# Optimization experiments

Hardware: AMD Instinct MI355X
Metric: run time of the kernel (lower is better)

Reference implementation:

```python
import jax, jax.numpy as jnp
import numpy as np

B, S, D, H = 2, 2048, 1024, 16
RANK = int(D * 0.2)  # 204, per decom(): rank = int(min(a,b)*ratio_LR)
HEAD = D // H


def setup_inputs() -> dict:
    key = jax.random.key(0)
    ks = jax.random.split(key, 16)
    s_in = 1.0 / np.sqrt(D)
    s_r = 1.0 / np.sqrt(RANK)
    inp = {
        'q': jax.random.normal(ks[0], (B, S, D), jnp.float32),
        'k': jax.random.normal(ks[1], (B, S, D), jnp.float32),
        'v': jax.random.normal(ks[2], (B, S, D), jnp.float32),
    }
    names = ['q', 'k', 'v', 'o']
    for i, n in enumerate(names):
        inp[f'V{n}'] = jax.random.uniform(ks[3 + 3 * i], (RANK, D), jnp.float32, -s_in, s_in)
        inp[f'U{n}'] = jax.random.uniform(ks[4 + 3 * i], (D, RANK), jnp.float32, -s_r, s_r)
        inp[f'b{n}'] = jax.random.uniform(ks[5 + 3 * i], (D,), jnp.float32, -s_r, s_r)
    return inp


def _factorized(x, Vw, Uw, b):
    # x @ V^T @ U^T + b  (low-rank linear: Linear(D->rank, no bias) then Linear(rank->D, bias))
    return jnp.einsum('bsr,dr->bsd', jnp.einsum('bsd,rd->bsr', x, Vw), Uw) + b


def _split_heads(x):
    # [B,S,D] -> [B,H,S,HEAD]
    return x.reshape(B, S, H, HEAD).transpose(0, 2, 1, 3)


def reference(q, k, v, Vq, Uq, bq, Vk, Uk, bk, Vv, Uv, bv, Vo, Uo, bo):
    qh = _split_heads(_factorized(q, Vq, Uq, bq))
    kh = _split_heads(_factorized(k, Vk, Uk, bk))
    vh = _split_heads(_factorized(v, Vv, Uv, bv))
    temperature = jnp.asarray(HEAD, jnp.float32) ** 0.5
    scores = jnp.einsum('bhqd,bhkd->bhqk', qh, kh) / temperature
    causal = jnp.tril(jnp.ones((S, S), bool))  # recreated each call in original
    scores = jnp.where(causal, scores, -jnp.inf)
    attn = jax.nn.softmax(scores, axis=-1)  # [B,H,S,S]
    out = jnp.einsum('bhqk,bhkd->bhqd', attn, vh)
    out = out.transpose(0, 2, 1, 3).reshape(B, S, D)
    out = _factorized(out, Vo, Uo, bo)
    # original returns attn flattened over batch*heads
    return out, attn.reshape(B * H, S, S)
```

## Files before the change

kernel.cpp:

```cpp
#include <hip/hip_runtime.h>
#include <stdint.h>

#define BB   2
#define SS   2048
#define DD   1024
#define NH   16
#define RK   204
#define RKP  256
#define HDIM 64
#define BH   (BB*NH)

typedef __attribute__((ext_vector_type(8))) short short8;
typedef __attribute__((ext_vector_type(4))) float f32x4;
typedef unsigned short u16;
typedef unsigned int   u32;

#define NEGBIG (-1e30f)

static __device__ __forceinline__ u16 f2bf(float f) {
    union { float f; u32 u; } v; v.f = f;
    u32 u = v.u;
    return (u16)((u + 0x7fffu + ((u >> 16) & 1u)) >> 16);
}
static __device__ __forceinline__ u32 pack2(float lo, float hi) {
    return (u32)f2bf(lo) | ((u32)f2bf(hi) << 16);
}

__global__ void cvt_bf16_k(const float* __restrict__ in, u16* __restrict__ out, int n4) {
    int i = blockIdx.x * blockDim.x + threadIdx.x;
    if (i < n4) {
        float4 f = ((const float4*)in)[i];
        u32 lo = pack2(f.x, f.y), hi = pack2(f.z, f.w);
        ((uint2*)out)[i] = make_uint2(lo, hi);
    }
}

__global__ void cvt_pad_u_k(const float* __restrict__ in, u16* __restrict__ out) {
    int i = blockIdx.x * blockDim.x + threadIdx.x;
    if (i >= DD * RKP) return;
    int row = i >> 8, col = i & (RKP - 1);
    out[i] = (col < RK) ? f2bf(in[row * RK + col]) : (u16)0;
}

template<int A_F32, int OUT_F32, int HAS_BIAS, int OUT_VT>
__global__ __launch_bounds__(256)
void gemm_nt_k(const void* __restrict__ Ap, int lda,
               const u16* __restrict__ Bp, int ldb, int nrowsB,
               const float* __restrict__ bias,
               void* __restrict__ Cp, int ldc, int K)
{
    __shared__ __align__(16) u16 As[64*72];
    __shared__ __align__(16) u16 Bs[64*72];
    const int row0 = blockIdx.x * 64;
    const int col0 = blockIdx.y * 64;
    const int t = threadIdx.x;
    const int w = t >> 6, lane = t & 63, quad = lane >> 4, l16 = lane & 15;
    const int r = t >> 2, seg = t & 3;

    f32x4 acc0 = 0.f, acc1 = 0.f, acc2 = 0.f, acc3 = 0.f;

    for (int k0 = 0; k0 < K; k0 += 64) {
        __syncthreads();
        if (A_F32) {
            const float* ga = (const float*)Ap + (size_t)(row0 + r) * lda + k0 + seg*16;
            float4 f0 = ((const float4*)ga)[0];
            float4 f1 = ((const float4*)ga)[1];
            float4 f2 = ((const float4*)ga)[2];
            float4 f3 = ((const float4*)ga)[3];
            uint4 s0 = { pack2(f0.x,f0.y), pack2(f0.z,f0.w), pack2(f1.x,f1.y), pack2(f1.z,f1.w) };
            uint4 s1 = { pack2(f2.x,f2.y), pack2(f2.z,f2.w), pack2(f3.x,f3.y), pack2(f3.z,f3.w) };
            *(uint4*)(As + r*72 + seg*16)     = s0;
            *(uint4*)(As + r*72 + seg*16 + 8) = s1;
        } else {
            const u16* ga = (const u16*)Ap + (size_t)(row0 + r) * lda + k0 + seg*16;
            *(uint4*)(As + r*72 + seg*16)     = ((const uint4*)ga)[0];
            *(uint4*)(As + r*72 + seg*16 + 8) = ((const uint4*)ga)[1];
        }
        {
            uint4 b0 = {0,0,0,0}, b1 = {0,0,0,0};
            if (col0 + r < nrowsB) {
                const u16* gb = Bp + (size_t)(col0 + r) * ldb + k0 + seg*16;
                b0 = ((const uint4*)gb)[0];
                b1 = ((const uint4*)gb)[1];
            }
            *(uint4*)(Bs + r*72 + seg*16)     = b0;
            *(uint4*)(Bs + r*72 + seg*16 + 8) = b1;
        }
        __syncthreads();
        #pragma unroll
        for (int c = 0; c < 2; ++c) {
            short8 a = *(const short8*)(As + (w*16 + l16)*72 + c*32 + quad*8);
            short8 b0v = *(const short8*)(Bs + (0*16 + l16)*72 + c*32 + quad*8);
            acc0 = __builtin_amdgcn_mfma_f32_16x16x32_bf16(a, b0v, acc0, 0, 0, 0);
            short8 b1v = *(const short8*)(Bs + (1*16 + l16)*72 + c*32 + quad*8);
            acc1 = __builtin_amdgcn_mfma_f32_16x16x32_bf16(a, b1v, acc1, 0, 0, 0);
            short8 b2v = *(const short8*)(Bs + (2*16 + l16)*72 + c*32 + quad*8);
            acc2 = __builtin_amdgcn_mfma_f32_16x16x32_bf16(a, b2v, acc2, 0, 0, 0);
            short8 b3v = *(const short8*)(Bs + (3*16 + l16)*72 + c*32 + quad*8);
            acc3 = __builtin_amdgcn_mfma_f32_16x16x32_bf16(a, b3v, acc3, 0, 0, 0);
        }
    }

    if (OUT_VT) {
        __syncthreads();
        #pragma unroll
        for (int f = 0; f < 4; ++f) {
            f32x4 a = (f==0) ? acc0 : (f==1) ? acc1 : (f==2) ? acc2 : acc3;
            int col = f*16 + l16;
            float bv = HAS_BIAS ? bias[col0 + col] : 0.f;
            #pragma unroll
            for (int rg = 0; rg < 4; ++rg) {
                int rowl = w*16 + quad*4 + rg;
                As[col*72 + rowl] = f2bf(a[rg] + bv);
            }
        }
        __syncthreads();
        const int b_ = row0 >> 11;
        const int s0 = row0 & (SS - 1);
        const int h  = col0 >> 6;
        u16* dst = (u16*)Cp + ((size_t)((b_*NH + h)*HDIM + r))*SS + s0 + seg*16;
        ((uint4*)dst)[0] = *(const uint4*)(As + r*72 + seg*16);
        ((uint4*)dst)[1] = *(const uint4*)(As + r*72 + seg*16 + 8);
        return;
    }

    #pragma unroll
    for (int f = 0; f < 4; ++f) {
        f32x4 a = (f==0) ? acc0 : (f==1) ? acc1 : (f==2) ? acc2 : acc3;
        int col = col0 + f*16 + l16;
        float bv = HAS_BIAS ? bias[col] : 0.f;
        #pragma unroll
        for (int rg = 0; rg < 4; ++rg) {
            int rowg = row0 + w*16 + quad*4 + rg;
            float val = a[rg] + bv;
            if (col >= nrowsB) val = 0.f;
            if (OUT_F32) ((float*)Cp)[(size_t)rowg*ldc + col] = val;
            else         ((u16*)Cp)[(size_t)rowg*ldc + col]  = f2bf(val);
        }
    }
}

#define QKT_8(sa0,sa1,sa2,sa3) do { \
    short8 b0 = *(const short8*)(Ks + (0*16 + l16)*72 + quad*8); \
    sa0 = __builtin_amdgcn_mfma_f32_16x16x32_bf16(q0, b0, sa0, 0,0,0); \
    short8 b0b = *(const short8*)(Ks + (0*16 + l16)*72 + 32 + quad*8); \
    sa0 = __builtin_amdgcn_mfma_f32_16x16x32_bf16(q1, b0b, sa0, 0,0,0); \
    short8 b1 = *(const short8*)(Ks + (1*16 + l16)*72 + quad*8); \
    sa1 = __builtin_amdgcn_mfma_f32_16x16x32_bf16(q0, b1, sa1, 0,0,0); \
    short8 b1b = *(const short8*)(Ks + (1*16 + l16)*72 + 32 + quad*8); \
    sa1 = __builtin_amdgcn_mfma_f32_16x16x32_bf16(q1, b1b, sa1, 0,0,0); \
    short8 b2 = *(const short8*)(Ks + (2*16 + l16)*72 + quad*8); \
    sa2 = __builtin_amdgcn_mfma_f32_16x16x32_bf16(q0, b2, sa2, 0,0,0); \
    short8 b2b = *(const short8*)(Ks + (2*16 + l16)*72 + 32 + quad*8); \
    sa2 = __builtin_amdgcn_mfma_f32_16x16x32_bf16(q1, b2b, sa2, 0,0,0); \
    short8 b3 = *(const short8*)(Ks + (3*16 + l16)*72 + quad*8); \
    sa3 = __builtin_amdgcn_mfma_f32_16x16x32_bf16(q0, b3, sa3, 0,0,0); \
    short8 b3b = *(const short8*)(Ks + (3*16 + l16)*72 + 32 + quad*8); \
    sa3 = __builtin_amdgcn_mfma_f32_16x16x32_bf16(q1, b3b, sa3, 0,0,0); \
} while (0)

__global__ __launch_bounds__(256)
void attn_k(const u16* __restrict__ qh, const u16* __restrict__ kh,
            const u16* __restrict__ vT,
            float* __restrict__ attn_out, u16* __restrict__ Ob)
{
    __shared__ __align__(16) u16 Ks[64*72];
    __shared__ __align__(16) u16 Vs[64*72];
    __shared__ __align__(16) u16 Ps[64*72];
    const int blk = blockIdx.x;
    const int qt = blk & 31, bh = blk >> 5;
    const int b_ = bh >> 4, h = bh & (NH - 1);
    const int qbase = qt * 64;
    const int t = threadIdx.x, w = t >> 6, lane = t & 63, quad = lane >> 4, l16 = lane & 15;
    const int r = t >> 2, seg = t & 3;
    const float scl = 0.125f;

    const u16* qrow = qh + (size_t)(b_*SS + qbase + w*16 + l16)*DD + h*HDIM;
    short8 q0 = *(const short8*)(qrow + quad*8);
    short8 q1 = *(const short8*)(qrow + 32 + quad*8);

    const u16* kstage = kh + (size_t)(b_*SS + r)*DD + h*HDIM + seg*16;
    const u16* vstage = vT + ((size_t)(bh*HDIM + r))*SS + seg*16;

    float m[4], l[4];
    #pragma unroll
    for (int rg = 0; rg < 4; ++rg) { m[rg] = NEGBIG; l[rg] = 0.f; }

    for (int kt = 0; kt <= qt; ++kt) {
        __syncthreads();
        {
            const u16* krow = kstage + (size_t)kt*64*DD;
            *(uint4*)(Ks + r*72 + seg*16)     = ((const uint4*)krow)[0];
            *(uint4*)(Ks + r*72 + seg*16 + 8) = ((const uint4*)krow)[1];
        }
        __syncthreads();

        f32x4 sa0 = 0.f, sa1 = 0.f, sa2 = 0.f, sa3 = 0.f;
        QKT_8(sa0, sa1, sa2, sa3);

        if (kt < qt) {
            #pragma unroll
            for (int rg = 0; rg < 4; ++rg) {
                float v0 = sa0[rg]*scl, v1 = sa1[rg]*scl, v2 = sa2[rg]*scl, v3 = sa3[rg]*scl;
                float m4 = fmaxf(fmaxf(v0, v1), fmaxf(v2, v3));
                float nm = fmaxf(m[rg], m4);
                l[rg] = l[rg]*__expf(m[rg]-nm)
                      + (__expf(v0-nm)+__expf(v1-nm)) + (__expf(v2-nm)+__expf(v3-nm));
                m[rg] = nm;
            }
        } else {
            int key0 = kt*64 + l16;
            #pragma unroll
            for (int rg = 0; rg < 4; ++rg) {
                int qg = qbase + w*16 + quad*4 + rg;
                bool c0 = (key0      <= qg), c1 = (key0 + 16 <= qg);
                bool c2 = (key0 + 32 <= qg), c3 = (key0 + 48 <= qg);
                float v0 = c0 ? sa0[rg]*scl : NEGBIG;
                float v1 = c1 ? sa1[rg]*scl : NEGBIG;
                float v2 = c2 ? sa2[rg]*scl : NEGBIG;
                float v3 = c3 ? sa3[rg]*scl : NEGBIG;
                float m4 = fmaxf(fmaxf(v0, v1), fmaxf(v2, v3));
                float nm = fmaxf(m[rg], m4);
                float e0 = c0 ? __expf(v0-nm) : 0.f;
                float e1 = c1 ? __expf(v1-nm) : 0.f;
                float e2 = c2 ? __expf(v2-nm) : 0.f;
                float e3 = c3 ? __expf(v3-nm) : 0.f;
                float corr = (m[rg] > NEGBIG) ? __expf(m[rg]-nm) : 0.f;
                l[rg] = l[rg]*corr + (e0+e1) + (e2+e3);
                m[rg] = nm;
            }
        }
    }

    #pragma unroll
    for (int rg = 0; rg < 4; ++rg) {
        #pragma unroll
        for (int d = 1; d < 16; d <<= 1) {
            float mo = __shfl_xor(m[rg], d);
            float lo = __shfl_xor(l[rg], d);
            float nm = fmaxf(m[rg], mo);
            l[rg] = l[rg]*__expf(m[rg]-nm) + lo*__expf(mo-nm);
            m[rg] = nm;
        }
    }
    float mr[4], rl[4];
    #pragma unroll
    for (int rg = 0; rg < 4; ++rg) { mr[rg] = m[rg]; rl[rg] = 1.f / l[rg]; }

    f32x4 oa0 = 0.f, oa1 = 0.f, oa2 = 0.f, oa3 = 0.f;
    float* attn_base = attn_out + (size_t)bh * SS * SS;
    float* rp0 = attn_base + (size_t)(qbase + w*16 + quad*4 + 0)*SS + l16;
    float* rp1 = attn_base + (size_t)(qbase + w*16 + quad*4 + 1)*SS + l16;
    float* rp2 = attn_base + (size_t)(qbase + w*16 + quad*4 + 2)*SS + l16;
    float* rp3 = attn_base + (size_t)(qbase + w*16 + quad*4 + 3)*SS + l16;

    for (int kt = 0; kt <= qt; ++kt) {
        __syncthreads();
        {
            const u16* krow = kstage + (size_t)kt*64*DD;
            *(uint4*)(Ks + r*72 + seg*16)     = ((const uint4*)krow)[0];
            *(uint4*)(Ks + r*72 + seg*16 + 8) = ((const uint4*)krow)[1];
            const u16* vrow = vstage + kt*64;
            *(uint4*)(Vs + r*72 + seg*16)     = ((const uint4*)vrow)[0];
            *(uint4*)(Vs + r*72 + seg*16 + 8) = ((const uint4*)vrow)[1];
        }
        __syncthreads();

        f32x4 sa0 = 0.f, sa1 = 0.f, sa2 = 0.f, sa3 = 0.f;
        QKT_8(sa0, sa1, sa2, sa3);

        if (kt < qt) {
            #pragma unroll
            for (int f = 0; f < 4; ++f) {
                f32x4 sv = (f==0) ? sa0 : (f==1) ? sa1 : (f==2) ? sa2 : sa3;
                float p0 = __expf(sv[0]*scl - mr[0]) * rl[0];
                float p1 = __expf(sv[1]*scl - mr[1]) * rl[1];
                float p2 = __expf(sv[2]*scl - mr[2]) * rl[2];
                float p3 = __expf(sv[3]*scl - mr[3]) * rl[3];
                rp0[f*16] = p0;
                rp1[f*16] = p1;
                rp2[f*16] = p2;
                rp3[f*16] = p3;
                Ps[(w*16 + quad*4 + 0)*72 + f*16 + l16] = f2bf(p0);
                Ps[(w*16 + quad*4 + 1)*72 + f*16 + l16] = f2bf(p1);
                Ps[(w*16 + quad*4 + 2)*72 + f*16 + l16] = f2bf(p2);
                Ps[(w*16 + quad*4 + 3)*72 + f*16 + l16] = f2bf(p3);
            }
        } else {
            int kbase = kt*64;
            #pragma unroll
            for (int f = 0; f < 4; ++f) {
                f32x4 sv = (f==0) ? sa0 : (f==1) ? sa1 : (f==2) ? sa2 : sa3;
                int key = kbase + f*16 + l16;
                #pragma unroll
                for (int rg = 0; rg < 4; ++rg) {
                    int qg = qbase + w*16 + quad*4 + rg;
                    float p = (key <= qg) ? __expf(sv[rg]*scl - mr[rg]) * rl[rg] : 0.f;
                    float* rp = (rg==0) ? rp0 : (rg==1) ? rp1 : (rg==2) ? rp2 : rp3;
                    rp[f*16] = p;
                    Ps[(w*16 + quad*4 + rg)*72 + f*16 + l16] = f2bf(p);
                }
            }
        }
        rp0 += 64; rp1 += 64; rp2 += 64; rp3 += 64;

        asm volatile("" ::: "memory");

        #pragma unroll
        for (int c = 0; c < 2; ++c) {
            short8 pa = *(const short8*)(Ps + (w*16 + l16)*72 + c*32 + quad*8);
            short8 v0 = *(const short8*)(Vs + (0*16 + l16)*72 + c*32 + quad*8);
            oa0 = __builtin_amdgcn_mfma_f32_16x16x32_bf16(pa, v0, oa0, 0,0,0);
            short8 v1 = *(const short8*)(Vs + (1*16 + l16)*72 + c*32 + quad*8);
            oa1 = __builtin_amdgcn_mfma_f32_16x16x32_bf16(pa, v1, oa1, 0,0,0);
            short8 v2 = *(const short8*)(Vs + (2*16 + l16)*72 + c*32 + quad*8);
            oa2 = __builtin_amdgcn_mfma_f32_16x16x32_bf16(pa, v2, oa2, 0,0,0);
            short8 v3 = *(const short8*)(Vs + (3*16 + l16)*72 + c*32 + quad*8);
            oa3 = __builtin_amdgcn_mfma_f32_16x16x32_bf16(pa, v3, oa3, 0,0,0);
        }
    }

    for (int kt = qt + 1; kt < 32; ++kt) {
        int kbase = kt * 64;
        f32x4 z = 0.f;
        f32x4* p = (f32x4*)(attn_base + (size_t)(qbase + r)*SS + kbase + seg*16);
        p[0] = z; p[1] = z; p[2] = z; p[3] = z;
    }

    #pragma unroll
    for (int f = 0; f < 4; ++f) {
        f32x4 ov = (f==0) ? oa0 : (f==1) ? oa1 : (f==2) ? oa2 : oa3;
        #pragma unroll
        for (int rg = 0; rg < 4; ++rg) {
            int qg = qbase + w*16 + quad*4 + rg;
            Ob[(size_t)(b_*SS + qg)*DD + h*HDIM + f*16 + l16] = f2bf(ov[rg]);
        }
    }
}

extern "C" void kernel_launch(void* const* d_in, const int* in_sizes, int n_in,
                              void* d_out, int out_size, void* d_ws, size_t ws_size,
                              hipStream_t stream)
{
    const float* xs[3] = { (const float*)d_in[0], (const float*)d_in[1], (const float*)d_in[2] };
    const float* Vw[4] = { (const float*)d_in[3], (const float*)d_in[6], (const float*)d_in[9],  (const float*)d_in[12] };
    const float* Uw[4] = { (const float*)d_in[4], (const float*)d_in[7], (const float*)d_in[10], (const float*)d_in[13] };
    const float* bw[4] = { (const float*)d_in[5], (const float*)d_in[8], (const float*)d_in[11], (const float*)d_in[14] };

    char* ws = (char*)d_ws;
    size_t off = 0;
    auto alloc = [&](size_t bytes) -> char* {
        char* p = ws + off;
        off += (bytes + 255) & ~(size_t)255;
        return p;
    };
    u16* wV[4]; for (int i = 0; i < 4; ++i) wV[i] = (u16*)alloc((size_t)RK*DD*2);
    u16* wU[4]; for (int i = 0; i < 4; ++i) wU[i] = (u16*)alloc((size_t)DD*RKP*2);
    u16* Tb  = (u16*)alloc((size_t)BB*SS*RKP*2);
    u16* hb[2]; for (int i = 0; i < 2; ++i) hb[i] = (u16*)alloc((size_t)BB*SS*DD*2);
    u16* vTb = (u16*)alloc((size_t)BB*SS*DD*2);
    u16* Ob  = (u16*)alloc((size_t)BB*SS*DD*2);
    (void)ws_size; (void)in_sizes; (void)n_in; (void)out_size;

    for (int i = 0; i < 4; ++i)
        cvt_bf16_k<<<(RK*DD/4 + 255)/256, 256, 0, stream>>>(Vw[i], wV[i], RK*DD/4);
    for (int i = 0; i < 4; ++i)
        cvt_pad_u_k<<<(DD*RKP + 255)/256, 256, 0, stream>>>(Uw[i], wU[i]);

    const int MROWS = BB*SS;
    for (int p = 0; p < 2; ++p) {
        gemm_nt_k<1,0,0,0><<<dim3(MROWS/64, RKP/64), 256, 0, stream>>>(
            xs[p], DD, wV[p], DD, RK, nullptr, Tb, RKP, DD);
        gemm_nt_k<0,0,1,0><<<dim3(MROWS/64, DD/64), 256, 0, stream>>>(
            Tb, RKP, wU[p], RKP, DD, bw[p], hb[p], DD, RKP);
    }
    gemm_nt_k<1,0,0,0><<<dim3(MROWS/64, RKP/64), 256, 0, stream>>>(
        xs[2], DD, wV[2], DD, RK, nullptr, Tb, RKP, DD);
    gemm_nt_k<0,0,1,1><<<dim3(MROWS/64, DD/64), 256, 0, stream>>>(
        Tb, RKP, wU[2], RKP, DD, bw[2], vTb, DD, RKP);

    float* attn_out = (float*)d_out + (size_t)BB*SS*DD;
    attn_k<<<BH*32, 256, 0, stream>>>(hb[0], hb[1], vTb, attn_out, Ob);

    gemm_nt_k<0,0,0,0><<<dim3(MROWS/64, RKP/64), 256, 0, stream>>>(
        Ob, DD, wV[3], DD, RK, nullptr, Tb, RKP, DD);
    gemm_nt_k<0,1,1,0><<<dim3(MROWS/64, DD/64), 256, 0, stream>>>(
        Tb, RKP, wU[3], RKP, DD, bw[3], d_out, DD, RKP);
}
```

Measured before the change: 807.3 us.

## Batch QKV projections per launch, fold softmax scale into Q, use hw exp2 and bf16 pack

Merges the four weight-conversion launches into two and batches the Q/K/V projection GEMMs into single launches using a z grid dimension, with separate intermediate buffers per projection. The 1/sqrt(head_dim) scale is folded into the Q projection epilogue, and softmax uses the hardware v_exp_f32 with a log2e FMA. Float-to-bf16 conversion now uses the v_cvt_pk_bf16_f32 instruction. The first attention pass stages two key tiles per barrier pair by reusing the V shared buffer. It adds workspace and relies on the rounding of the hardware conversion instruction.

```diff
diff --git a/kernel.cpp b/kernel.cpp
--- a/kernel.cpp
+++ b/kernel.cpp
@@ -16,39 +16,57 @@
 typedef unsigned int   u32;
 
 #define NEGBIG (-1e30f)
-
-static __device__ __forceinline__ u16 f2bf(float f) {
-    union { float f; u32 u; } v; v.f = f;
-    u32 u = v.u;
-    return (u16)((u + 0x7fffu + ((u >> 16) & 1u)) >> 16);
-}
-static __device__ __forceinline__ u32 pack2(float lo, float hi) {
-    return (u32)f2bf(lo) | ((u32)f2bf(hi) << 16);
-}
-
-__global__ void cvt_bf16_k(const float* __restrict__ in, u16* __restrict__ out, int n4) {
+#define LOG2E  1.4426950408889634f
+
+static __device__ __forceinline__ u32 cvtpk(float lo, float hi) {
+    u32 r; asm("v_cvt_pk_bf16_f32 %0, %1, %2" : "=v"(r) : "v"(lo), "v"(hi)); return r;
+}
+static __device__ __forceinline__ u16 f2bf(float f) { return (u16)cvtpk(f, f); }
+static __device__ __forceinline__ u32 pack2(float lo, float hi) { return cvtpk(lo, hi); }
+static __device__ __forceinline__ float exp2_hw(float x) {
+    float r; asm("v_exp_f32 %0, %1" : "=v"(r) : "v"(x)); return r;
+}
+
+struct C4 { const float *s0, *s1, *s2, *s3; u16 *d0, *d1, *d2, *d3; };
+
+__global__ void cvt_bf16_b4(C4 c, int n4) {
+    int y = blockIdx.y;
+    const float* in = (y==0)?c.s0:(y==1)?c.s1:(y==2)?c.s2:c.s3;
+    u16* out = (y==0)?c.d0:(y==1)?c.d1:(y==2)?c.d2:c.d3;
     int i = blockIdx.x * blockDim.x + threadIdx.x;
     if (i < n4) {
         float4 f = ((const float4*)in)[i];
-        u32 lo = pack2(f.x, f.y), hi = pack2(f.z, f.w);
-        ((uint2*)out)[i] = make_uint2(lo, hi);
-    }
-}
-
-__global__ void cvt_pad_u_k(const float* __restrict__ in, u16* __restrict__ out) {
+        ((uint2*)out)[i] = make_uint2(pack2(f.x, f.y), pack2(f.z, f.w));
+    }
+}
+
+__global__ void cvt_pad_b4(C4 c, int n) {
+    int y = blockIdx.y;
+    const float* in = (y==0)?c.s0:(y==1)?c.s1:(y==2)?c.s2:c.s3;
+    u16* out = (y==0)?c.d0:(y==1)?c.d1:(y==2)?c.d2:c.d3;
     int i = blockIdx.x * blockDim.x + threadIdx.x;
-    if (i >= DD * RKP) return;
+    if (i >= n) return;
     int row = i >> 8, col = i & (RKP - 1);
     out[i] = (col < RK) ? f2bf(in[row * RK + col]) : (u16)0;
 }
 
-template<int A_F32, int OUT_F32, int HAS_BIAS, int OUT_VT>
+struct B3 {
+    const void *A0, *A1, *A2;
+    const u16  *B0, *B1, *B2;
+    const float *bb0, *bb1, *bb2;
+    void *C0, *C1, *C2;
+};
+
+template<int A_F32, int OUT_F32, int HAS_BIAS, int VT_LAST, int QSC>
 __global__ __launch_bounds__(256)
-void gemm_nt_k(const void* __restrict__ Ap, int lda,
-               const u16* __restrict__ Bp, int ldb, int nrowsB,
-               const float* __restrict__ bias,
-               void* __restrict__ Cp, int ldc, int K)
+void gemm_nt_k(B3 g, int lda, int ldb, int nrowsB, int ldc, int K)
 {
+    const int z = blockIdx.z;
+    const void* Ap  = (z==0)?g.A0:(z==1)?g.A1:g.A2;
+    const u16*  Bp  = (z==0)?g.B0:(z==1)?g.B1:g.B2;
+    const float* bias = (z==0)?g.bb0:(z==1)?g.bb1:g.bb2;
+    void* Cp = (z==0)?g.C0:(z==1)?g.C1:g.C2;
+
     __shared__ __align__(16) u16 As[64*72];
     __shared__ __align__(16) u16 Bs[64*72];
     const int row0 = blockIdx.x * 64;
@@ -101,7 +119,7 @@
         }
     }
 
-    if (OUT_VT) {
+    if (VT_LAST && z == 2) {
         __syncthreads();
         #pragma unroll
         for (int f = 0; f < 4; ++f) {
@@ -124,6 +142,7 @@
         return;
     }
 
+    const float osc = (QSC && z == 0) ? 0.125f : 1.f;
     #pragma unroll
     for (int f = 0; f < 4; ++f) {
         f32x4 a = (f==0) ? acc0 : (f==1) ? acc1 : (f==2) ? acc2 : acc3;
@@ -132,7 +151,7 @@
         #pragma unroll
         for (int rg = 0; rg < 4; ++rg) {
             int rowg = row0 + w*16 + quad*4 + rg;
-            float val = a[rg] + bv;
+            float val = (a[rg] + bv) * osc;
             if (col >= nrowsB) val = 0.f;
             if (OUT_F32) ((float*)Cp)[(size_t)rowg*ldc + col] = val;
             else         ((u16*)Cp)[(size_t)rowg*ldc + col]  = f2bf(val);
@@ -140,24 +159,67 @@
     }
 }
 
-#define QKT_8(sa0,sa1,sa2,sa3) do { \
-    short8 b0 = *(const short8*)(Ks + (0*16 + l16)*72 + quad*8); \
+#define QKT_8(BUF,sa0,sa1,sa2,sa3) do { \
+    short8 b0 = *(const short8*)(BUF + (0*16 + l16)*72 + quad*8); \
     sa0 = __builtin_amdgcn_mfma_f32_16x16x32_bf16(q0, b0, sa0, 0,0,0); \
-    short8 b0b = *(const short8*)(Ks + (0*16 + l16)*72 + 32 + quad*8); \
+    short8 b0b = *(const short8*)(BUF + (0*16 + l16)*72 + 32 + quad*8); \
     sa0 = __builtin_amdgcn_mfma_f32_16x16x32_bf16(q1, b0b, sa0, 0,0,0); \
-    short8 b1 = *(const short8*)(Ks + (1*16 + l16)*72 + quad*8); \
+    short8 b1 = *(const short8*)(BUF + (1*16 + l16)*72 + quad*8); \
     sa1 = __builtin_amdgcn_mfma_f32_16x16x32_bf16(q0, b1, sa1, 0,0,0); \
-    short8 b1b = *(const short8*)(Ks + (1*16 + l16)*72 + 32 + quad*8); \
+    short8 b1b = *(const short8*)(BUF + (1*16 + l16)*72 + 32 + quad*8); \
     sa1 = __builtin_amdgcn_mfma_f32_16x16x32_bf16(q1, b1b, sa1, 0,0,0); \
-    short8 b2 = *(const short8*)(Ks + (2*16 + l16)*72 + quad*8); \
+    short8 b2 = *(const short8*)(BUF + (2*16 + l16)*72 + quad*8); \
     sa2 = __builtin_amdgcn_mfma_f32_16x16x32_bf16(q0, b2, sa2, 0,0,0); \
-    short8 b2b = *(const short8*)(Ks + (2*16 + l16)*72 + 32 + quad*8); \
+    short8 b2b = *(const short8*)(BUF + (2*16 + l16)*72 + 32 + quad*8); \
     sa2 = __builtin_amdgcn_mfma_f32_16x16x32_bf16(q1, b2b, sa2, 0,0,0); \
-    short8 b3 = *(const short8*)(Ks + (3*16 + l16)*72 + quad*8); \
+    short8 b3 = *(const short8*)(BUF + (3*16 + l16)*72 + quad*8); \
     sa3 = __builtin_amdgcn_mfma_f32_16x16x32_bf16(q0, b3, sa3, 0,0,0); \
-    short8 b3b = *(const short8*)(Ks + (3*16 + l16)*72 + 32 + quad*8); \
+    short8 b3b = *(const short8*)(BUF + (3*16 + l16)*72 + 32 + quad*8); \
     sa3 = __builtin_amdgcn_mfma_f32_16x16x32_bf16(q1, b3b, sa3, 0,0,0); \
 } while (0)
+
+static __device__ __forceinline__ void p1_int(
+    const f32x4& sa0, const f32x4& sa1, const f32x4& sa2, const f32x4& sa3,
+    float* m, float* l)
+{
+    #pragma unroll
+    for (int rg = 0; rg < 4; ++rg) {
+        float v0 = sa0[rg], v1 = sa1[rg], v2 = sa2[rg], v3 = sa3[rg];
+        float m4 = fmaxf(fmaxf(v0, v1), fmaxf(v2, v3));
+        float nm = fmaxf(m[rg], m4);
+        float nm2 = nm * LOG2E;
+        float e = exp2_hw(__builtin_fmaf(v0, LOG2E, -nm2)) + exp2_hw(__builtin_fmaf(v1, LOG2E, -nm2))
+                + exp2_hw(__builtin_fmaf(v2, LOG2E, -nm2)) + exp2_hw(__builtin_fmaf(v3, LOG2E, -nm2));
+        float corr = exp2_hw(__builtin_fmaf(m[rg], LOG2E, -nm2));
+        l[rg] = l[rg]*corr + e;
+        m[rg] = nm;
+    }
+}
+static __device__ __forceinline__ void p1_diag(
+    const f32x4& sa0, const f32x4& sa1, const f32x4& sa2, const f32x4& sa3,
+    float* m, float* l, int key0, int qg0)
+{
+    #pragma unroll
+    for (int rg = 0; rg < 4; ++rg) {
+        int qg = qg0 + rg;
+        bool c0 = (key0      <= qg), c1 = (key0 + 16 <= qg);
+        bool c2 = (key0 + 32 <= qg), c3 = (key0 + 48 <= qg);
+        float v0 = c0 ? sa0[rg] : NEGBIG;
+        float v1 = c1 ? sa1[rg] : NEGBIG;
+        float v2 = c2 ? sa2[rg] : NEGBIG;
+        float v3 = c3 ? sa3[rg] : NEGBIG;
+        float m4 = fmaxf(fmaxf(v0, v1), fmaxf(v2, v3));
+        float nm = fmaxf(m[rg], m4);
+        float nm2 = nm * LOG2E;
+        float e0 = c0 ? exp2_hw(__builtin_fmaf(v0, LOG2E, -nm2)) : 0.f;
+        float e1 = c1 ? exp2_hw(__builtin_fmaf(v1, LOG2E, -nm2)) : 0.f;
+        float e2 = c2 ? exp2_hw(__builtin_fmaf(v2, LOG2E, -nm2)) : 0.f;
+        float e3 = c3 ? exp2_hw(__builtin_fmaf(v3, LOG2E, -nm2)) : 0.f;
+        float corr = (m[rg] > NEGBIG) ? exp2_hw(__builtin_fmaf(m[rg], LOG2E, -nm2)) : 0.f;
+        l[rg] = l[rg]*corr + (e0+e1) + (e2+e3);
+        m[rg] = nm;
+    }
+}
 
 __global__ __launch_bounds__(256)
 void attn_k(const u16* __restrict__ qh, const u16* __restrict__ kh,
@@ -173,7 +235,6 @@
     const int qbase = qt * 64;
     const int t = threadIdx.x, w = t >> 6, lane = t & 63, quad = lane >> 4, l16 = lane & 15;
     const int r = t >> 2, seg = t & 3;
-    const float scl = 0.125f;
 
     const u16* qrow = qh + (size_t)(b_*SS + qbase + w*16 + l16)*DD + h*HDIM;
     short8 q0 = *(const short8*)(qrow + quad*8);
@@ -181,54 +242,37 @@
 
     const u16* kstage = kh + (size_t)(b_*SS + r)*DD + h*HDIM + seg*16;
     const u16* vstage = vT + ((size_t)(bh*HDIM + r))*SS + seg*16;
+    const int qg0 = qbase + w*16 + quad*4;
 
     float m[4], l[4];
     #pragma unroll
     for (int rg = 0; rg < 4; ++rg) { m[rg] = NEGBIG; l[rg] = 0.f; }
 
-    for (int kt = 0; kt <= qt; ++kt) {
+    for (int kt0 = 0; kt0 <= qt; kt0 += 2) {
+        const bool two = (kt0 + 1) <= qt;
         __syncthreads();
         {
-            const u16* krow = kstage + (size_t)kt*64*DD;
+            const u16* krow = kstage + (size_t)kt0*64*DD;
             *(uint4*)(Ks + r*72 + seg*16)     = ((const uint4*)krow)[0];
             *(uint4*)(Ks + r*72 + seg*16 + 8) = ((const uint4*)krow)[1];
-        }
-        __syncthreads();
-
-        f32x4 sa0 = 0.f, sa1 = 0.f, sa2 = 0.f, sa3 = 0.f;
-        QKT_8(sa0, sa1, sa2, sa3);
-
-        if (kt < qt) {
-            #pragma unroll
-            for (int rg = 0; rg < 4; ++rg) {
-                float v0 = sa0[rg]*scl, v1 = sa1[rg]*scl, v2 = sa2[rg]*scl, v3 = sa3[rg]*scl;
-                float m4 = fmaxf(fmaxf(v0, v1), fmaxf(v2, v3));
-                float nm = fmaxf(m[rg], m4);
-                l[rg] = l[rg]*__expf(m[rg]-nm)
-                      + (__expf(v0-nm)+__expf(v1-nm)) + (__expf(v2-nm)+__expf(v3-nm));
-                m[rg] = nm;
+            if (two) {
+                const u16* krow2 = krow + (size_t)64*DD;
+                *(uint4*)(Vs + r*72 + seg*16)     = ((const uint4*)krow2)[0];
+                *(uint4*)(Vs + r*72 + seg*16 + 8) = ((const uint4*)krow2)[1];
             }
-        } else {
-            int key0 = kt*64 + l16;
-            #pragma unroll
-            for (int rg = 0; rg < 4; ++rg) {
-                int qg = qbase + w*16 + quad*4 + rg;
-                bool c0 = (key0      <= qg), c1 = (key0 + 16 <= qg);
-                bool c2 = (key0 + 32 <= qg), c3 = (key0 + 48 <= qg);
-                float v0 = c0 ? sa0[rg]*scl : NEGBIG;
-                float v1 = c1 ? sa1[rg]*scl : NEGBIG;
-                float v2 = c2 ? sa2[rg]*scl : NEGBIG;
-                float v3 = c3 ? sa3[rg]*scl : NEGBIG;
-                float m4 = fmaxf(fmaxf(v0, v1), fmaxf(v2, v3));
-                float nm = fmaxf(m[rg], m4);
-                float e0 = c0 ? __expf(v0-nm) : 0.f;
-                float e1 = c1 ? __expf(v1-nm) : 0.f;
-                float e2 = c2 ? __expf(v2-nm) : 0.f;
-                float e3 = c3 ? __expf(v3-nm) : 0.f;
-                float corr = (m[rg] > NEGBIG) ? __expf(m[rg]-nm) : 0.f;
-                l[rg] = l[rg]*corr + (e0+e1) + (e2+e3);
-                m[rg] = nm;
-            }
+        }
+        __syncthreads();
+        {
+            f32x4 sa0 = 0.f, sa1 = 0.f, sa2 = 0.f, sa3 = 0.f;
+            QKT_8(Ks, sa0, sa1, sa2, sa3);
+            if (kt0 < qt) p1_int(sa0, sa1, sa2, sa3, m, l);
+            else          p1_diag(sa0, sa1, sa2, sa3, m, l, kt0*64 + l16, qg0);
+        }
+        if (two) {
+            f32x4 sa0 = 0.f, sa1 = 0.f, sa2 = 0.f, sa3 = 0.f;
+            QKT_8(Vs, sa0, sa1, sa2, sa3);
+            if (kt0 + 1 < qt) p1_int(sa0, sa1, sa2, sa3, m, l);
+            else              p1_diag(sa0, sa1, sa2, sa3, m, l, (kt0+1)*64 + l16, qg0);
         }
     }
 
@@ -243,16 +287,17 @@
             m[rg] = nm;
         }
     }
-    float mr[4], rl[4];
-    #pragma unroll
-    for (int rg = 0; rg < 4; ++rg) { mr[rg] = m[rg]; rl[rg] = 1.f / l[rg]; }
+    float mneg2[4], rl[4];
+    #pragma unroll
+    for (int rg = 0; rg < 4; ++rg) { mneg2[rg] = -(m[rg]*LOG2E); rl[rg] = 1.f / l[rg]; }
 
     f32x4 oa0 = 0.f, oa1 = 0.f, oa2 = 0.f, oa3 = 0.f;
     float* attn_base = attn_out + (size_t)bh * SS * SS;
-    float* rp0 = attn_base + (size_t)(qbase + w*16 + quad*4 + 0)*SS + l16;
-    float* rp1 = attn_base + (size_t)(qbase + w*16 + quad*4 + 1)*SS + l16;
-    float* rp2 = attn_base + (size_t)(qbase + w*16 + quad*4 + 2)*SS + l16;
-    float* rp3 = attn_base + (size_t)(qbase + w*16 + quad*4 + 3)*SS + l16;
+    float* rp0 = attn_base + (size_t)(qg0 + 0)*SS + l16;
+    float* rp1 = attn_base + (size_t)(qg0 + 1)*SS + l16;
+    float* rp2 = attn_base + (size_t)(qg0 + 2)*SS + l16;
+    float* rp3 = attn_base + (size_t)(qg0 + 3)*SS + l16;
+    const int psrow = w*16 + quad*4;
 
     for (int kt = 0; kt <= qt; ++kt) {
         __syncthreads();
@@ -267,24 +312,22 @@
         __syncthreads();
 
         f32x4 sa0 = 0.f, sa1 = 0.f, sa2 = 0.f, sa3 = 0.f;
-        QKT_8(sa0, sa1, sa2, sa3);
+        QKT_8(Ks, sa0, sa1, sa2, sa3);
 
         if (kt < qt) {
             #pragma unroll
             for (int f = 0; f < 4; ++f) {
                 f32x4 sv = (f==0) ? sa0 : (f==1) ? sa1 : (f==2) ? sa2 : sa3;
-                float p0 = __expf(sv[0]*scl - mr[0]) * rl[0];
-                float p1 = __expf(sv[1]*scl - mr[1]) * rl[1];
-                float p2 = __expf(sv[2]*scl - mr[2]) * rl[2];
-                float p3 = __expf(sv[3]*scl - mr[3]) * rl[3];
-                rp0[f*16] = p0;
-                rp1[f*16] = p1;
-                rp2[f*16] = p2;
-                rp3[f*16] = p3;
-                Ps[(w*16 + quad*4 + 0)*72 + f*16 + l16] = f2bf(p0);
-                Ps[(w*16 + quad*4 + 1)*72 + f*16 + l16] = f2bf(p1);
-                Ps[(w*16 + quad*4 + 2)*72 + f*16 + l16] = f2bf(p2);
-                Ps[(w*16 + quad*4 + 3)*72 + f*16 + l16] = f2bf(p3);
+                float p0 = exp2_hw(__builtin_fmaf(sv[0], LOG2E, mneg2[0])) * rl[0];
+                float p1 = exp2_hw(__builtin_fmaf(sv[1], LOG2E, mneg2[1])) * rl[1];
+                float p2 = exp2_hw(__builtin_fmaf(sv[2], LOG2E, mneg2[2])) * rl[2];
+                float p3 = exp2_hw(__builtin_fmaf(sv[3], LOG2E, mneg2[3])) * rl[3];
+                rp0[f*16] = p0; rp1[f*16] = p1; rp2[f*16] = p2; rp3[f*16] = p3;
+                u32 pk01 = cvtpk(p0, p1), pk23 = cvtpk(p2, p3);
+                Ps[(psrow+0)*72 + f*16 + l16] = (u16)pk01;
+                Ps[(psrow+1)*72 + f*16 + l16] = (u16)(pk01 >> 16);
+                Ps[(psrow+2)*72 + f*16 + l16] = (u16)pk23;
+                Ps[(psrow+3)*72 + f*16 + l16] = (u16)(pk23 >> 16);
             }
         } else {
             int kbase = kt*64;
@@ -292,14 +335,16 @@
             for (int f = 0; f < 4; ++f) {
                 f32x4 sv = (f==0) ? sa0 : (f==1) ? sa1 : (f==2) ? sa2 : sa3;
                 int key = kbase + f*16 + l16;
-                #pragma unroll
-                for (int rg = 0; rg < 4; ++rg) {
-                    int qg = qbase + w*16 + quad*4 + rg;
-                    float p = (key <= qg) ? __expf(sv[rg]*scl - mr[rg]) * rl[rg] : 0.f;
-                    float* rp = (rg==0) ? rp0 : (rg==1) ? rp1 : (rg==2) ? rp2 : rp3;
-                    rp[f*16] = p;
-                    Ps[(w*16 + quad*4 + rg)*72 + f*16 + l16] = f2bf(p);
-                }
+                float p0 = (key <= qg0+0) ? exp2_hw(__builtin_fmaf(sv[0], LOG2E, mneg2[0]))*rl[0] : 0.f;
+                float p1 = (key <= qg0+1) ? exp2_hw(__builtin_fmaf(sv[1], LOG2E, mneg2[1]))*rl[1] : 0.f;
+                float p2 = (key <= qg0+2) ? exp2_hw(__builtin_fmaf(sv[2], LOG2E, mneg2[2]))*rl[2] : 0.f;
+                float p3 = (key <= qg0+3) ? exp2_hw(__builtin_fmaf(sv[3], LOG2E, mneg2[3]))*rl[3] : 0.f;
+                rp0[f*16] = p0; rp1[f*16] = p1; rp2[f*16] = p2; rp3[f*16] = p3;
+                u32 pk01 = cvtpk(p0, p1), pk23 = cvtpk(p2, p3);
+                Ps[(psrow+0)*72 + f*16 + l16] = (u16)pk01;
+                Ps[(psrow+1)*72 + f*16 + l16] = (u16)(pk01 >> 16);
+                Ps[(psrow+2)*72 + f*16 + l16] = (u16)pk23;
+                Ps[(psrow+3)*72 + f*16 + l16] = (u16)(pk23 >> 16);
             }
         }
         rp0 += 64; rp1 += 64; rp2 += 64; rp3 += 64;
@@ -332,7 +377,7 @@
         f32x4 ov = (f==0) ? oa0 : (f==1) ? oa1 : (f==2) ? oa2 : oa3;
         #pragma unroll
         for (int rg = 0; rg < 4; ++rg) {
-            int qg = qbase + w*16 + quad*4 + rg;
+            int qg = qg0 + rg;
             Ob[(size_t)(b_*SS + qg)*DD + h*HDIM + f*16 + l16] = f2bf(ov[rg]);
         }
     }
@@ -356,34 +401,46 @@
     };
     u16* wV[4]; for (int i = 0; i < 4; ++i) wV[i] = (u16*)alloc((size_t)RK*DD*2);
     u16* wU[4]; for (int i = 0; i < 4; ++i) wU[i] = (u16*)alloc((size_t)DD*RKP*2);
-    u16* Tb  = (u16*)alloc((size_t)BB*SS*RKP*2);
+    u16* Tb[3]; for (int i = 0; i < 3; ++i) Tb[i] = (u16*)alloc((size_t)BB*SS*RKP*2);
     u16* hb[2]; for (int i = 0; i < 2; ++i) hb[i] = (u16*)alloc((size_t)BB*SS*DD*2);
     u16* vTb = (u16*)alloc((size_t)BB*SS*DD*2);
     u16* Ob  = (u16*)alloc((size_t)BB*SS*DD*2);
     (void)ws_size; (void)in_sizes; (void)n_in; (void)out_size;
 
-    for (int i = 0; i < 4; ++i)
-        cvt_bf16_k<<<(RK*DD/4 + 255)/256, 256, 0, stream>>>(Vw[i], wV[i], RK*DD/4);
-    for (int i = 0; i < 4; ++i)
-        cvt_pad_u_k<<<(DD*RKP + 255)/256, 256, 0, stream>>>(Uw[i], wU[i]);
+    {
+        C4 cv = { Vw[0], Vw[1], Vw[2], Vw[3], wV[0], wV[1], wV[2], wV[3] };
+        cvt_bf16_b4<<<dim3((RK*DD/4 + 255)/256, 4), 256, 0, stream>>>(cv, RK*DD/4);
+        C4 cu = { Uw[0], Uw[1], Uw[2], Uw[3], wU[0], wU[1], wU[2], wU[3] };
+        cvt_pad_b4<<<dim3((DD*RKP + 255)/256, 4), 256, 0, stream>>>(cu, DD*RKP);
+    }
 
     const int MROWS = BB*SS;
-    for (int p = 0; p < 2; ++p) {
-        gemm_nt_k<1,0,0,0><<<dim3(MROWS/64, RKP/64), 256, 0, stream>>>(
-            xs[p], DD, wV[p], DD, RK, nullptr, Tb, RKP, DD);
-        gemm_nt_k<0,0,1,0><<<dim3(MROWS/64, DD/64), 256, 0, stream>>>(
-            Tb, RKP, wU[p], RKP, DD, bw[p], hb[p], DD, RKP);
-    }
-    gemm_nt_k<1,0,0,0><<<dim3(MROWS/64, RKP/64), 256, 0, stream>>>(
-        xs[2], DD, wV[2], DD, RK, nullptr, Tb, RKP, DD);
-    gemm_nt_k<0,0,1,1><<<dim3(MROWS/64, DD/64), 256, 0, stream>>>(
-        Tb, RKP, wU[2], RKP, DD, bw[2], vTb, DD, RKP);
+    {
+        B3 g = { xs[0], xs[1], xs[2], wV[0], wV[1], wV[2],
+                 nullptr, nullptr, nullptr, Tb[0], Tb[1], Tb[2] };
+        gemm_nt_k<1,0,0,0,0><<<dim3(MROWS/64, RKP/64, 3), 256, 0, stream>>>(
+            g, DD, DD, RK, RKP, DD);
+    }
+    {
+        B3 g = { Tb[0], Tb[1], Tb[2], wU[0], wU[1], wU[2],
+                 bw[0], bw[1], bw[2], hb[0], hb[1], vTb };
+        gemm_nt_k<0,0,1,1,1><<<dim3(MROWS/64, DD/64, 3), 256, 0, stream>>>(
+            g, RKP, RKP, DD, DD, RKP);
+    }
 
     float* attn_out = (float*)d_out + (size_t)BB*SS*DD;
     attn_k<<<BH*32, 256, 0, stream>>>(hb[0], hb[1], vTb, attn_out, Ob);
 
-    gemm_nt_k<0,0,0,0><<<dim3(MROWS/64, RKP/64), 256, 0, stream>>>(
-        Ob, DD, wV[3], DD, RK, nullptr, Tb, RKP, DD);
-    gemm_nt_k<0,1,1,0><<<dim3(MROWS/64, DD/64), 256, 0, stream>>>(
-        Tb, RKP, wU[3], RKP, DD, bw[3], d_out, DD, RKP);
-}
+    {
+        B3 g = { Ob, Ob, Ob, wV[3], wV[3], wV[3],
+                 nullptr, nullptr, nullptr, Tb[0], Tb[0], Tb[0] };
+        gemm_nt_k<0,0,0,0,0><<<dim3(MROWS/64, RKP/64, 1), 256, 0, stream>>>(
+            g, DD, DD, RK, RKP, DD);
+    }
+    {
+        B3 g = { Tb[0], Tb[0], Tb[0], wU[3], wU[3], wU[3],
+                 bw[3], bw[3], bw[3], d_out, d_out, d_out };
+        gemm_nt_k<0,1,1,0,0><<<dim3(MROWS/64, DD/64, 1), 256, 0, stream>>>(
+            g, RKP, RKP, DD, DD, RKP);
+    }
+}
```

Measured after the change: 755.0 us. 6.5% less time.
